# Kernel optimization log

Measured on AMD Instinct MI355X. Metric: run time of the kernel, lower is better.

## Reference

```python
import jax, jax.numpy as jnp
import numpy as np

RES = 128
RANK = 8
PE_L = 6
ENC = 256
N = 1 << 20
IN_DIM = RANK + 3 + 3 * 2 * PE_L  # 47


def _linear_init(key, fan_in, fan_out):
    kw, kb = jax.random.split(key)
    bound = 1.0 / np.sqrt(fan_in)
    W = jax.random.uniform(kw, (fan_in, fan_out), jnp.float32, -bound, bound)
    b = jax.random.uniform(kb, (fan_out,), jnp.float32, -bound, bound)
    return W, b


def setup_inputs() -> dict:
    key = jax.random.key(0)
    ks = jax.random.split(key, 12)
    x = jax.random.uniform(ks[0], (N, 3), jnp.float32, -1.0, 1.0)
    f_xy = jax.random.normal(ks[1], (RANK, RES, RES), jnp.float32)
    f_xz = jax.random.normal(ks[2], (RANK, RES, RES), jnp.float32)
    f_yz = jax.random.normal(ks[3], (RANK, RES, RES), jnp.float32)
    W0, b0 = _linear_init(ks[4], IN_DIM, ENC)
    W1, b1 = _linear_init(ks[5], ENC, ENC)
    W2, b2 = _linear_init(ks[6], ENC, ENC)
    W3, b3 = _linear_init(ks[7], ENC, ENC)
    W_sig, b_sig = _linear_init(ks[8], ENC, 1)
    W_rgb, b_rgb = _linear_init(ks[9], ENC, 3)
    return {
        "x": x, "f_xy": f_xy, "f_xz": f_xz, "f_yz": f_yz,
        "W0": W0, "b0": b0, "W1": W1, "b1": b1,
        "W2": W2, "b2": b2, "W3": W3, "b3": b3,
        "W_sig": W_sig, "b_sig": b_sig, "W_rgb": W_rgb, "b_rgb": b_rgb,
    }


def reference(x, f_xy, f_xz, f_yz, W0, b0, W1, b1, W2, b2, W3, b3,
              W_sig, b_sig, W_rgb, b_rgb):
    # map [-1,1] coords to voxel indices (truncation like .long(), then clamp)
    coords = (x + 1.0) * 0.5 * (RES - 1)
    idx = jnp.clip(coords.astype(jnp.int32), 0, RES - 1)
    ix, iy, iz = idx[:, 0], idx[:, 1], idx[:, 2]
    # tri-planar CP-factor gathers: each [rank, N]
    feat = (f_xy[:, iy, ix] + f_xz[:, iz, ix] + f_yz[:, iz, iy]).T  # [N, rank]
    # positional encoding: [x, (sin(2^l x), cos(2^l x)) for l in 0..L-1]
    freqs = 2.0 ** jnp.arange(PE_L, dtype=jnp.float32)          # [L]
    ang = x[:, None, :] * freqs[None, :, None]                   # [N, L, 3]
    pe_sc = jnp.concatenate([jnp.sin(ang), jnp.cos(ang)], axis=-1)  # [N, L, 6]
    pe = jnp.concatenate([x, pe_sc.reshape(x.shape[0], -1)], axis=-1)  # [N, 3+6L]
    h = jnp.concatenate([feat, pe], axis=-1)                     # [N, 47]
    for W, b in ((W0, b0), (W1, b1), (W2, b2), (W3, b3)):
        h = jax.nn.relu(h @ W + b)
    sigma = jax.nn.softplus(h @ W_sig + b_sig)                   # [N, 1]
    rgb = jax.nn.sigmoid(h @ W_rgb + b_rgb)                      # [N, 3]
    return (rgb, sigma)
```

## Files before the change

kernel.cpp:

```cpp
#include <hip/hip_runtime.h>
#include <hip/hip_bf16.h>

typedef unsigned short ushort_t;
typedef unsigned int uint_t;
typedef unsigned char uchar_t;

typedef float f32x4 __attribute__((ext_vector_type(4)));
typedef float f32x16 __attribute__((ext_vector_type(16)));

#define NPTS (1 << 20)

#define OFF_FLAG 0
#define OFF_B0   16
#define OFF_B1   272
#define OFF_B2   528
#define OFF_B3   784
#define OFF_BSIG 1040
#define OFF_BRGB 1041
#define OFF_W0   1056
#define OFF_W1   9248
#define OFF_W2   42016
#define OFF_W3   74784
#define OFF_WH   107552
#define OFF_PL   111648

__device__ __forceinline__ float bf2f(ushort_t u) {
  union { uint_t i; float f; } c; c.i = ((uint_t)u) << 16; return c.f;
}
__device__ __forceinline__ ushort_t f2bf(float f) {
  union { float f; uint_t i; } c; c.f = f;
  uint_t x = c.i;
  return (ushort_t)((x + 0x7fffu + ((x >> 16) & 1u)) >> 16);
}
__device__ __forceinline__ uint_t f2fp8b_soft(float x) {
  union { float f; uint_t u; } v; v.f = x;
  uint_t s = (v.u >> 24) & 0x80u;
  float ax = fabsf(x);
  if (ax < 0.015625f) return s | (uint_t)(int)rintf(ax * 512.0f);
  if (ax >= 448.0f) return s | 0x7Eu;
  int e2; float m = frexpf(ax, &e2);
  int q = (int)rintf(m * 16.0f) - 8;
  int e = e2 - 1;
  if (q == 8) { q = 0; ++e; }
  if (e == 8 && q > 6) q = 6;
  return s | ((uint_t)(e + 7) << 3) | (uint_t)q;
}

#if defined(__has_builtin)
#if __has_builtin(__builtin_amdgcn_cvt_pk_fp8_f32)
#define HAVE_HW_FP8 1
#endif
#endif

#ifdef HAVE_HW_FP8
__device__ __forceinline__ uint_t pk4fp8(float a, float b, float c, float d) {
  uint_t r = (uint_t)__builtin_amdgcn_cvt_pk_fp8_f32(a, b, 0, false);
  r = (uint_t)__builtin_amdgcn_cvt_pk_fp8_f32(c, d, r, true);
  return r;
}
__device__ __forceinline__ uchar_t f2fp8(float x) {
  return (uchar_t)(__builtin_amdgcn_cvt_pk_fp8_f32(x, 0.0f, 0, false) & 0xFFu);
}
#else
__device__ __forceinline__ uint_t pk4fp8(float a, float b, float c, float d) {
  return f2fp8b_soft(a) | (f2fp8b_soft(b) << 8) | (f2fp8b_soft(c) << 16) | (f2fp8b_soft(d) << 24);
}
__device__ __forceinline__ uchar_t f2fp8(float x) { return (uchar_t)f2fp8b_soft(x); }
#endif

__device__ __forceinline__ float ldf(const void* p, long i, int isbf) {
  return isbf ? bf2f(((const ushort_t*)p)[i]) : ((const float*)p)[i];
}
__device__ __forceinline__ ushort_t ldbf(const void* p, long i, int isbf) {
  return isbf ? ((const ushort_t*)p)[i] : f2bf(((const float*)p)[i]);
}
__device__ __forceinline__ void stf(void* p, long i, int isbf, float v) {
  if (isbf) ((ushort_t*)p)[i] = f2bf(v);
  else      ((float*)p)[i] = v;
}

__device__ __forceinline__ int fp8addr(int p, int k) {
  return ((p >> 5) << 13) + ((k >> 4) << 9) + (((k >> 3) & 1) << 8)
       + ((p & 31) << 3) + (k & 7);
}

union UA { uint2 u; long l; };

__global__ void sniff_dtype(const void* __restrict__ f, ushort_t* __restrict__ ws) {
  __shared__ int s_cnt;
  if (threadIdx.x == 0) s_cnt = 0;
  __syncthreads();
  const ushort_t* u = (const ushort_t*)f;
  int c = 0;
  for (int j = 0; j < 4; ++j) {
    ushort_t v = u[(threadIdx.x * 4 + j) * 2];
    int e = (v >> 7) & 0xFF;
    if (e > 100 && e < 140) ++c;
  }
  atomicAdd(&s_cnt, c);
  __syncthreads();
  if (threadIdx.x == 0) ((uint_t*)ws)[0] = (s_cnt >= 160) ? 1u : 0u;
}

__global__ void prep_bias(const void* __restrict__ b0, const void* __restrict__ b1,
                          const void* __restrict__ b2, const void* __restrict__ b3,
                          const void* __restrict__ bsig, const void* __restrict__ brgb,
                          ushort_t* __restrict__ ws) {
  const int isbf = (int)((const uint_t*)ws)[0];
  int i = threadIdx.x;
  ws[OFF_B0 + i] = ldbf(b0, i, isbf);
  ws[OFF_B1 + i] = ldbf(b1, i, isbf);
  ws[OFF_B2 + i] = ldbf(b2, i, isbf);
  ws[OFF_B3 + i] = ldbf(b3, i, isbf);
  if (i == 0) ws[OFF_BSIG] = ldbf(bsig, 0, isbf);
  if (i < 3) ws[OFF_BRGB + i] = ldbf(brgb, i, isbf);
}

__global__ void prep_weights(const void* __restrict__ W0,
                             const void* __restrict__ W1,
                             const void* __restrict__ W2,
                             const void* __restrict__ W3,
                             const void* __restrict__ Wsig,
                             const void* __restrict__ Wrgb,
                             ushort_t* __restrict__ ws) {
  const int isbf = (int)((const uint_t*)ws)[0];
  int t = blockIdx.x * 256 + threadIdx.x;
  if (t >= 432 * 64) return;
  int lane = t & 63;
  int tile = t >> 6;
  const void* src = nullptr;
  ushort_t* dst;
  int local, Ksrc = 256;
  bool head = false;
  if (tile < 32) { local = tile; src = W0; Ksrc = 47; dst = ws + OFF_W0 + (size_t)local * 256; }
  else if (tile < 160) { local = tile - 32;  src = W1; dst = ws + OFF_W1 + (size_t)local * 256; }
  else if (tile < 288) { local = tile - 160; src = W2; dst = ws + OFF_W2 + (size_t)local * 256; }
  else if (tile < 416) { local = tile - 288; src = W3; dst = ws + OFF_W3 + (size_t)local * 256; }
  else { local = tile - 416; head = true; dst = ws + OFF_WH + (size_t)local * 256; }
  int kt = head ? local : (local >> 3);
  int mt = head ? 0 : (local & 7);
  int n = mt * 32 + (lane & 31);
  int kb = kt * 16 + (lane >> 5) * 8;
  for (int j = 0; j < 8; j += 4) {
    float v[4];
    for (int jj = 0; jj < 4; ++jj) {
      int k = kb + j + jj;
      float vv = 0.0f;
      if (head) {
        if (n < 3) vv = ldf(Wrgb, (long)k * 3 + n, isbf);
        else if (n == 3) vv = ldf(Wsig, k, isbf);
      } else if (k < Ksrc) {
        vv = ldf(src, (long)k * 256 + n, isbf);
      }
      v[jj] = vv * 16.0f;
    }
    uint_t pk = pk4fp8(v[0], v[1], v[2], v[3]);
    dst[lane * 4 + (j >> 1)]     = (ushort_t)(pk & 0xFFFFu);
    dst[lane * 4 + (j >> 1) + 1] = (ushort_t)(pk >> 16);
  }
}

__global__ void prep_planes(const void* __restrict__ fxy,
                            const void* __restrict__ fxz,
                            const void* __restrict__ fyz,
                            ushort_t* __restrict__ ws) {
  const int isbf = (int)((const uint_t*)ws)[0];
  int t = blockIdx.x * 256 + threadIdx.x;
  int plane = t >> 14, pos = t & 16383;
  const void* src = (plane == 0) ? fxy : (plane == 1) ? fxz : fyz;
  ushort_t* d = ws + OFF_PL + (size_t)plane * 131072 + (size_t)pos * 8;
  for (int r = 0; r < 8; ++r) d[r] = ldbf(src, (long)r * 16384 + pos, isbf);
}

template <int KT>
__device__ __forceinline__ void mlp_layer(uchar_t* s_act,
                                          const uchar_t* __restrict__ wsW,
                                          const uchar_t* __restrict__ nextW,
                                          const ushort_t* __restrict__ bias,
                                          int w, int lane, UA (&a)[4][2]) {
  f32x16 acc[2][4] = {};
  const int p31 = lane & 31;
  const int q2 = lane >> 5;
  const uchar_t* bptr = s_act + lane * 8;
  const uchar_t* aptr = wsW + w * 1024 + lane * 8;
  const uchar_t* nptr = nextW + w * 1024 + lane * 8;
  UA b[2][4];
#pragma unroll
  for (int d = 0; d < 4; ++d) b[0][d].u = *(const uint2*)(bptr + d * 8192);
#pragma unroll 1
  for (int g = 0; g < KT / 4 - 1; ++g) {
    const uchar_t* ag = aptr + g * 16384;
    const uchar_t* bg = bptr + g * 2048;
#pragma unroll
    for (int j = 0; j < 4; ++j) {
#pragma unroll
      for (int d = 0; d < 4; ++d)
        b[(j + 1) & 1][d].u = *(const uint2*)(bg + (j + 1) * 512 + d * 8192);
#pragma unroll
      for (int mi = 0; mi < 2; ++mi)
#pragma unroll
        for (int d = 0; d < 4; ++d)
          acc[mi][d] = __builtin_amdgcn_mfma_f32_32x32x16_fp8_fp8(a[j][mi].l, b[j & 1][d].l, acc[mi][d], 0, 0, 0);
#pragma unroll
      for (int mi = 0; mi < 2; ++mi)
        a[j][mi].u = *(const uint2*)(ag + 16384 + j * 4096 + mi * 512);
    }
  }
  {
    const uchar_t* bg = bptr + (KT / 4 - 1) * 2048;
#pragma unroll
    for (int j = 0; j < 4; ++j) {
      if (j < 3) {
#pragma unroll
        for (int d = 0; d < 4; ++d)
          b[(j + 1) & 1][d].u = *(const uint2*)(bg + (j + 1) * 512 + d * 8192);
      }
#pragma unroll
      for (int mi = 0; mi < 2; ++mi)
#pragma unroll
        for (int d = 0; d < 4; ++d)
          acc[mi][d] = __builtin_amdgcn_mfma_f32_32x32x16_fp8_fp8(a[j][mi].l, b[j & 1][d].l, acc[mi][d], 0, 0, 0);
#pragma unroll
      for (int mi = 0; mi < 2; ++mi)
        a[j][mi].u = *(const uint2*)(nptr + j * 4096 + mi * 512);
    }
  }
  __syncthreads();
  uchar_t* wbase = s_act + w * 2048 + p31 * 8 + q2 * 4;
#pragma unroll
  for (int mi = 0; mi < 2; ++mi) {
#pragma unroll
    for (int rq = 0; rq < 4; ++rq) {
      int col0 = w * 64 + mi * 32 + rq * 8 + q2 * 4;
      ushort4 bb = *(const ushort4*)(bias + col0);
      float bf0 = bf2f(bb.x), bf1 = bf2f(bb.y), bf2v = bf2f(bb.z), bf3 = bf2f(bb.w);
#pragma unroll
      for (int d = 0; d < 4; ++d) {
        const f32x16& A = acc[mi][d];
        float v0 = fmaxf(fmaf(A[rq * 4 + 0], 0.0625f, bf0), 0.0f);
        float v1 = fmaxf(fmaf(A[rq * 4 + 1], 0.0625f, bf1), 0.0f);
        float v2 = fmaxf(fmaf(A[rq * 4 + 2], 0.0625f, bf2v), 0.0f);
        float v3 = fmaxf(fmaf(A[rq * 4 + 3], 0.0625f, bf3), 0.0f);
        *(uint_t*)(wbase + d * 8192 + mi * 1024 + (rq >> 1) * 512 + (rq & 1) * 256)
            = pk4fp8(v0, v1, v2, v3);
      }
    }
  }
  __syncthreads();
}

__global__ __launch_bounds__(256, 2)
void tensorf_main(const void* __restrict__ x,
                  const ushort_t* __restrict__ ws,
                  void* __restrict__ out) {
  __shared__ uchar_t s_act[4 * 16 * 512];
  const int isbf = (int)((const uint_t*)ws)[0];
  const int tid = threadIdx.x;
  const int lane = tid & 63;
  const int wid = tid >> 6;
  const int blk = blockIdx.x;

  UA a[4][2];
  {
    const uchar_t* a0 = (const uchar_t*)(ws + OFF_W0) + wid * 1024 + lane * 8;
#pragma unroll
    for (int t = 0; t < 4; ++t)
#pragma unroll
      for (int mi = 0; mi < 2; ++mi)
        a[t][mi].u = *(const uint2*)(a0 + t * 4096 + mi * 512);
  }

  {
    int pl = tid >> 1;
    int s = tid & 1;
    long p = (long)blk * 128 + pl;
    float x0 = ldf(x, p * 3 + 0, isbf);
    float x1 = ldf(x, p * 3 + 1, isbf);
    float x2 = ldf(x, p * 3 + 2, isbf);
    float fx[3] = { x0, x1, x2 };
    if (s == 0) {
      int ix = (int)(((x0 + 1.0f) * 0.5f) * 127.0f);
      int iy = (int)(((x1 + 1.0f) * 0.5f) * 127.0f);
      int iz = (int)(((x2 + 1.0f) * 0.5f) * 127.0f);
      ix = ix < 0 ? 0 : (ix > 127 ? 127 : ix);
      iy = iy < 0 ? 0 : (iy > 127 ? 127 : iy);
      iz = iz < 0 ? 0 : (iz > 127 ? 127 : iz);
      union { uint4 u; ushort_t s[8]; } a4, b4, c4;
      a4.u = *(const uint4*)(ws + OFF_PL + (size_t)(iy * 128 + ix) * 8);
      b4.u = *(const uint4*)(ws + OFF_PL + 131072 + (size_t)(iz * 128 + ix) * 8);
      c4.u = *(const uint4*)(ws + OFF_PL + 262144 + (size_t)(iz * 128 + iy) * 8);
      float fv[8];
#pragma unroll
      for (int r = 0; r < 8; ++r)
        fv[r] = bf2f(a4.s[r]) + bf2f(b4.s[r]) + bf2f(c4.s[r]);
      uint2 f;
      f.x = pk4fp8(fv[0], fv[1], fv[2], fv[3]);
      f.y = pk4fp8(fv[4], fv[5], fv[6], fv[7]);
      *(uint2*)(s_act + fp8addr(pl, 0)) = f;
      s_act[fp8addr(pl, 8)]  = f2fp8(x0);
      s_act[fp8addr(pl, 9)]  = f2fp8(x1);
      s_act[fp8addr(pl, 10)] = f2fp8(x2);
#pragma unroll
      for (int l = 4; l < 6; ++l) {
        float fr = (float)(1 << l);
        int k0 = 11 + l * 6;
#pragma unroll
        for (int dd = 0; dd < 3; ++dd) {
          float ang = fx[dd] * fr;
          s_act[fp8addr(pl, k0 + dd)]     = f2fp8(__sinf(ang));
          s_act[fp8addr(pl, k0 + 3 + dd)] = f2fp8(__cosf(ang));
        }
      }
      s_act[fp8addr(pl, 47)] = 0;
      *(uint2*)(s_act + fp8addr(pl, 48)) = uint2{0u, 0u};
      *(uint2*)(s_act + fp8addr(pl, 56)) = uint2{0u, 0u};
    } else {
#pragma unroll
      for (int l = 0; l < 4; ++l) {
        float fr = (float)(1 << l);
        int k0 = 11 + l * 6;
#pragma unroll
        for (int dd = 0; dd < 3; ++dd) {
          float ang = fx[dd] * fr;
          s_act[fp8addr(pl, k0 + dd)]     = f2fp8(__sinf(ang));
          s_act[fp8addr(pl, k0 + 3 + dd)] = f2fp8(__cosf(ang));
        }
      }
    }
  }
  __syncthreads();

  const uchar_t* w0 = (const uchar_t*)(ws + OFF_W0);
  const uchar_t* w1 = (const uchar_t*)(ws + OFF_W1);
  const uchar_t* w2 = (const uchar_t*)(ws + OFF_W2);
  const uchar_t* w3 = (const uchar_t*)(ws + OFF_W3);
  const uchar_t* wh = (const uchar_t*)(ws + OFF_WH);
  mlp_layer<4>(s_act,  w0, w1, ws + OFF_B0, wid, lane, a);
  mlp_layer<16>(s_act, w1, w2, ws + OFF_B1, wid, lane, a);
  mlp_layer<16>(s_act, w2, w3, ws + OFF_B2, wid, lane, a);
  mlp_layer<16>(s_act, w3, wh, ws + OFF_B3, wid, lane, a);

  {
    f32x16 acc = {};
    const int p31 = lane & 31;
    const int q2 = lane >> 5;
    const uchar_t* hb = s_act + wid * 8192 + lane * 8;
    const uchar_t* whp = wh + lane * 8;
#pragma unroll 4
    for (int kt = 0; kt < 16; ++kt) {
      UA ta, tb;
      ta.u = *(const uint2*)(whp + kt * 512);
      tb.u = *(const uint2*)(hb + kt * 512);
      acc = __builtin_amdgcn_mfma_f32_32x32x16_fp8_fp8(ta.l, tb.l, acc, 0, 0, 0);
    }
    if (q2 == 0) {
      long pp = (long)blk * 128 + wid * 32 + p31;
      float br0 = bf2f(ws[OFF_BRGB + 0]), br1 = bf2f(ws[OFF_BRGB + 1]), br2 = bf2f(ws[OFF_BRGB + 2]);
      float bs = bf2f(ws[OFF_BSIG]);
      float z0 = fmaf(acc[0], 0.0625f, br0);
      float z1 = fmaf(acc[1], 0.0625f, br1);
      float z2 = fmaf(acc[2], 0.0625f, br2);
      stf(out, pp * 3 + 0, isbf, 1.0f / (1.0f + __expf(-z0)));
      stf(out, pp * 3 + 1, isbf, 1.0f / (1.0f + __expf(-z1)));
      stf(out, pp * 3 + 2, isbf, 1.0f / (1.0f + __expf(-z2)));
      float zs = fmaf(acc[3], 0.0625f, bs);
      float sp = (zs > 20.0f) ? zs : __logf(1.0f + __expf(zs));
      stf(out, (long)3 * NPTS + pp, isbf, sp);
    }
  }
}

extern "C" void kernel_launch(void* const* d_in, const int* in_sizes, int n_in,
                              void* d_out, int out_size, void* d_ws, size_t ws_size,
                              hipStream_t stream) {
  const void* x    = d_in[0];
  const void* fxy  = d_in[1];
  const void* fxz  = d_in[2];
  const void* fyz  = d_in[3];
  const void* W0   = d_in[4];
  const void* b0   = d_in[5];
  const void* W1   = d_in[6];
  const void* b1   = d_in[7];
  const void* W2   = d_in[8];
  const void* b2   = d_in[9];
  const void* W3   = d_in[10];
  const void* b3   = d_in[11];
  const void* Wsig = d_in[12];
  const void* bsig = d_in[13];
  const void* Wrgb = d_in[14];
  const void* brgb = d_in[15];
  ushort_t* ws = (ushort_t*)d_ws;

  hipLaunchKernelGGL(sniff_dtype, dim3(1), dim3(64), 0, stream, fxy, ws);
  hipLaunchKernelGGL(prep_bias, dim3(1), dim3(256), 0, stream,
                     b0, b1, b2, b3, bsig, brgb, ws);
  hipLaunchKernelGGL(prep_weights, dim3(108), dim3(256), 0, stream,
                     W0, W1, W2, W3, Wsig, Wrgb, ws);
  hipLaunchKernelGGL(prep_planes, dim3(192), dim3(256), 0, stream,
                     fxy, fxz, fyz, ws);
  hipLaunchKernelGGL(tensorf_main, dim3(8192), dim3(256), 0, stream,
                     x, ws, d_out);
}
```

Measured before the change: 440.9 us.

## Use MX-scaled 32x32x64 FP8 MFMA with double-buffered weight fragments

Replaces groups of four 32x32x16 FP8 MFMAs with a single scaled 32x32x64 f8f6f4 MFMA (unit scales), packing four 8-byte fragments into an 8-int operand. The layer loop is restructured so a full K-group of weights for the next group or next layer is prefetched into a ping-pong register buffer, and activations are loaded per output column block with double buffering. The aim is to cut MFMA issue count and use the higher-throughput MX instruction on gfx950. In exchange it needs more registers per operand, and relies on the K ordering of the concatenated fragments matching the wider instruction's layout.

```diff
diff --git a/kernel.cpp b/kernel.cpp
--- a/kernel.cpp
+++ b/kernel.cpp
@@ -7,6 +7,7 @@
 
 typedef float f32x4 __attribute__((ext_vector_type(4)));
 typedef float f32x16 __attribute__((ext_vector_type(16)));
+typedef int v8i __attribute__((ext_vector_type(8)));
 
 #define NPTS (1 << 20)
 
@@ -50,6 +51,9 @@
 #if __has_builtin(__builtin_amdgcn_cvt_pk_fp8_f32)
 #define HAVE_HW_FP8 1
 #endif
+#if __has_builtin(__builtin_amdgcn_mfma_scale_f32_32x32x64_f8f6f4)
+#define HAVE_MX 1
+#endif
 #endif
 
 #ifdef HAVE_HW_FP8
@@ -68,6 +72,20 @@
 __device__ __forceinline__ uchar_t f2fp8(float x) { return (uchar_t)f2fp8b_soft(x); }
 #endif
 
+union AU { v8i v; uint2 u2[4]; long l[4]; };
+
+__device__ __forceinline__ f32x16 mx_mfma(const AU& A, const AU& B, f32x16 C) {
+#ifdef HAVE_MX
+  return __builtin_amdgcn_mfma_scale_f32_32x32x64_f8f6f4(
+      A.v, B.v, C, 0, 0, 0, (int)0x7F7F7F7F, 0, (int)0x7F7F7F7F);
+#else
+#pragma unroll
+  for (int s = 0; s < 4; ++s)
+    C = __builtin_amdgcn_mfma_f32_32x32x16_fp8_fp8(A.l[s], B.l[s], C, 0, 0, 0);
+  return C;
+#endif
+}
+
 __device__ __forceinline__ float ldf(const void* p, long i, int isbf) {
   return isbf ? bf2f(((const ushort_t*)p)[i]) : ((const float*)p)[i];
 }
@@ -83,8 +101,6 @@
   return ((p >> 5) << 13) + ((k >> 4) << 9) + (((k >> 3) & 1) << 8)
        + ((p & 31) << 3) + (k & 7);
 }
-
-union UA { uint2 u; long l; };
 
 __global__ void sniff_dtype(const void* __restrict__ f, ushort_t* __restrict__ ws) {
   __shared__ int s_cnt;
@@ -172,57 +188,41 @@
   for (int r = 0; r < 8; ++r) d[r] = ldbf(src, (long)r * 16384 + pos, isbf);
 }
 
-template <int KT>
+template <int KT, int CUR>
 __device__ __forceinline__ void mlp_layer(uchar_t* s_act,
                                           const uchar_t* __restrict__ wsW,
                                           const uchar_t* __restrict__ nextW,
                                           const ushort_t* __restrict__ bias,
-                                          int w, int lane, UA (&a)[4][2]) {
+                                          int w, int lane, AU (&a)[2][2]) {
+  constexpr int G = KT / 4;
   f32x16 acc[2][4] = {};
   const int p31 = lane & 31;
   const int q2 = lane >> 5;
   const uchar_t* bptr = s_act + lane * 8;
   const uchar_t* aptr = wsW + w * 1024 + lane * 8;
   const uchar_t* nptr = nextW + w * 1024 + lane * 8;
-  UA b[2][4];
-#pragma unroll
-  for (int d = 0; d < 4; ++d) b[0][d].u = *(const uint2*)(bptr + d * 8192);
-#pragma unroll 1
-  for (int g = 0; g < KT / 4 - 1; ++g) {
-    const uchar_t* ag = aptr + g * 16384;
+  AU b[2];
+#pragma unroll
+  for (int g = 0; g < G; ++g) {
+    const int c = (CUR + g) & 1;
+    const uchar_t* ap = (g + 1 < G) ? (aptr + (size_t)(g + 1) * 16384) : nptr;
+#pragma unroll
+    for (int mi = 0; mi < 2; ++mi)
+#pragma unroll
+      for (int s = 0; s < 4; ++s)
+        a[c ^ 1][mi].u2[s] = *(const uint2*)(ap + s * 4096 + mi * 512);
     const uchar_t* bg = bptr + g * 2048;
 #pragma unroll
-    for (int j = 0; j < 4; ++j) {
-#pragma unroll
-      for (int d = 0; d < 4; ++d)
-        b[(j + 1) & 1][d].u = *(const uint2*)(bg + (j + 1) * 512 + d * 8192);
-#pragma unroll
-      for (int mi = 0; mi < 2; ++mi)
-#pragma unroll
-        for (int d = 0; d < 4; ++d)
-          acc[mi][d] = __builtin_amdgcn_mfma_f32_32x32x16_fp8_fp8(a[j][mi].l, b[j & 1][d].l, acc[mi][d], 0, 0, 0);
-#pragma unroll
-      for (int mi = 0; mi < 2; ++mi)
-        a[j][mi].u = *(const uint2*)(ag + 16384 + j * 4096 + mi * 512);
-    }
-  }
-  {
-    const uchar_t* bg = bptr + (KT / 4 - 1) * 2048;
-#pragma unroll
-    for (int j = 0; j < 4; ++j) {
-      if (j < 3) {
-#pragma unroll
-        for (int d = 0; d < 4; ++d)
-          b[(j + 1) & 1][d].u = *(const uint2*)(bg + (j + 1) * 512 + d * 8192);
-      }
-#pragma unroll
-      for (int mi = 0; mi < 2; ++mi)
-#pragma unroll
-        for (int d = 0; d < 4; ++d)
-          acc[mi][d] = __builtin_amdgcn_mfma_f32_32x32x16_fp8_fp8(a[j][mi].l, b[j & 1][d].l, acc[mi][d], 0, 0, 0);
-#pragma unroll
-      for (int mi = 0; mi < 2; ++mi)
-        a[j][mi].u = *(const uint2*)(nptr + j * 4096 + mi * 512);
+    for (int s = 0; s < 4; ++s) b[0].u2[s] = *(const uint2*)(bg + s * 512);
+#pragma unroll
+    for (int d = 0; d < 4; ++d) {
+      if (d < 3) {
+#pragma unroll
+        for (int s = 0; s < 4; ++s)
+          b[(d + 1) & 1].u2[s] = *(const uint2*)(bg + (d + 1) * 8192 + s * 512);
+      }
+      acc[0][d] = mx_mfma(a[c][0], b[d & 1], acc[0][d]);
+      acc[1][d] = mx_mfma(a[c][1], b[d & 1], acc[1][d]);
     }
   }
   __syncthreads();
@@ -260,14 +260,14 @@
   const int wid = tid >> 6;
   const int blk = blockIdx.x;
 
-  UA a[4][2];
+  AU a[2][2];
   {
     const uchar_t* a0 = (const uchar_t*)(ws + OFF_W0) + wid * 1024 + lane * 8;
 #pragma unroll
-    for (int t = 0; t < 4; ++t)
-#pragma unroll
-      for (int mi = 0; mi < 2; ++mi)
-        a[t][mi].u = *(const uint2*)(a0 + t * 4096 + mi * 512);
+    for (int mi = 0; mi < 2; ++mi)
+#pragma unroll
+      for (int s = 0; s < 4; ++s)
+        a[0][mi].u2[s] = *(const uint2*)(a0 + s * 4096 + mi * 512);
   }
 
   {
@@ -335,10 +335,10 @@
   const uchar_t* w2 = (const uchar_t*)(ws + OFF_W2);
   const uchar_t* w3 = (const uchar_t*)(ws + OFF_W3);
   const uchar_t* wh = (const uchar_t*)(ws + OFF_WH);
-  mlp_layer<4>(s_act,  w0, w1, ws + OFF_B0, wid, lane, a);
-  mlp_layer<16>(s_act, w1, w2, ws + OFF_B1, wid, lane, a);
-  mlp_layer<16>(s_act, w2, w3, ws + OFF_B2, wid, lane, a);
-  mlp_layer<16>(s_act, w3, wh, ws + OFF_B3, wid, lane, a);
+  mlp_layer<4, 0>(s_act,  w0, w1, ws + OFF_B0, wid, lane, a);
+  mlp_layer<16, 1>(s_act, w1, w2, ws + OFF_B1, wid, lane, a);
+  mlp_layer<16, 1>(s_act, w2, w3, ws + OFF_B2, wid, lane, a);
+  mlp_layer<16, 1>(s_act, w3, wh, ws + OFF_B3, wid, lane, a);
 
   {
     f32x16 acc = {};
@@ -346,12 +346,15 @@
     const int q2 = lane >> 5;
     const uchar_t* hb = s_act + wid * 8192 + lane * 8;
     const uchar_t* whp = wh + lane * 8;
-#pragma unroll 4
-    for (int kt = 0; kt < 16; ++kt) {
-      UA ta, tb;
-      ta.u = *(const uint2*)(whp + kt * 512);
-      tb.u = *(const uint2*)(hb + kt * 512);
-      acc = __builtin_amdgcn_mfma_f32_32x32x16_fp8_fp8(ta.l, tb.l, acc, 0, 0, 0);
+    AU ta, tb;
+#pragma unroll
+    for (int g = 0; g < 4; ++g) {
+#pragma unroll
+      for (int s = 0; s < 4; ++s) {
+        ta.u2[s] = *(const uint2*)(whp + (size_t)(4 * g + s) * 512);
+        tb.u2[s] = *(const uint2*)(hb + (size_t)(4 * g + s) * 512);
+      }
+      acc = mx_mfma(ta, tb, acc);
     }
     if (q2 == 0) {
       long pp = (long)blk * 128 + wid * 32 + p31;
```

After: 355.1 us. 19.5% less time.
